# Kernel optimization log

Measured on AMD Instinct MI355X. Metric: run time of the kernel, lower is better.

Reference implementation:

```python
import jax, jax.numpy as jnp
import numpy as np

EPS = 1e-7
NUM_HEADS = 16

def _ln(x, g, b):
    m = jnp.mean(x, -1, keepdims=True)
    v = jnp.var(x, -1, keepdims=True)
    return (x - m) * jax.lax.rsqrt(v + EPS) * g + b

def _gelu(x):
    return jax.nn.gelu(x, approximate=False)  # torch nn.GELU default = exact erf

def _attn(x, qkv_w, qkv_b, pw, pb):
    B, N, C = x.shape
    D = C // NUM_HEADS
    qkv = (x @ qkv_w.T + qkv_b).reshape(B, N, 3, NUM_HEADS, D).transpose(2, 0, 3, 1, 4)
    q, k, v = qkv[0], qkv[1], qkv[2]
    a = jax.nn.softmax(jnp.einsum('bhnd,bhmd->bhnm', q, k) * (D ** -0.5), axis=-1)
    o = jnp.einsum('bhnm,bhmd->bhnd', a, v).transpose(0, 2, 1, 3).reshape(B, N, C)
    return o @ pw.T + pb

def _gcn(x, w, b, adj):
    # x: (B,C,J); w: (C*K,C) 1x1 conv, then einsum 'nkctv,kvw->nctw' with t==1
    K = adj.shape[0]
    B, C, J = x.shape
    y = jnp.einsum('bcj,oc->boj', x, w) + b[None, :, None]
    y = y.reshape(B, K, C, J)
    return jnp.einsum('bkcv,kvw->bcw', y, adj)

def _mlp(x, w1, b1, w2, b2):
    return _gelu(_gelu(x @ w1.T + b1) @ w2.T + b2)

def _lrsc(x, adj, l1g, l1b, l2g, l2b, g1w, g1b, g2w, g2b, m1w, m1b, m2w, m2b):
    x = x.transpose(0, 2, 1)                       # (B,C,J)
    res = x
    xn = _ln(x, l1g, l1b)                          # LayerNorm over J
    x = res + _mlp(xn, m1w, m1b, m2w, m2b) + _gcn(xn, g1w, g1b, adj)
    x = _ln(x.transpose(0, 2, 1), l2g, l2b).transpose(0, 2, 1)  # LayerNorm over C
    res = x
    x = res + _mlp(x, m1w, m1b, m2w, m2b) + _gcn(x, g2w, g2b, adj)
    return x.transpose(0, 2, 1)                    # (B,J,C)

def _gkpc(x, lg, lb, q1w, q1b, p1w, p1b, q2w, q2b, p2w, p2b):
    x = x + _attn(_ln(x, lg, lb), q1w, q1b, p1w, p1b)
    return _attn(_ln(x, lg, lb), q2w, q2b, p2w, p2b)  # note: no residual on second attn

def _forward(x, adj, ln1_g, ln1_b, ln2_g, ln2_b, gcn1_w, gcn1_b, gcn2_w, gcn2_b,
             mlp1_w1, mlp1_b1, mlp1_w2, mlp1_b2, attn_ln_g, attn_ln_b,
             qkv1_w, qkv1_b, proj1_w, proj1_b, qkv2_w, qkv2_b, proj2_w, proj2_b,
             tn_g, tn_b):
    L = ln1_g.shape[0]
    for i in range(L):
        # GG_ACM/RR_ACM/LCM are published as identity -> both 0.3/0.7 mixes equal x + gelu(x)
        xin = x + _gelu(x)
        x5 = _gkpc(xin, attn_ln_g[i], attn_ln_b[i], qkv1_w[i], qkv1_b[i],
                   proj1_w[i], proj1_b[i], qkv2_w[i], qkv2_b[i], proj2_w[i], proj2_b[i])
        x7 = _lrsc(xin, adj, ln1_g[i], ln1_b[i], ln2_g[i], ln2_b[i],
                   gcn1_w[i], gcn1_b[i], gcn2_w[i], gcn2_b[i],
                   mlp1_w1[i], mlp1_b1[i], mlp1_w2[i], mlp1_b2[i])
        x = x + x5 + x7
    return _ln(x, tn_g, tn_b)

def setup_inputs():
    B, V, C, K, L = 2048, 17, 512, 3, 3
    s = 0.05
    ks = jax.random.split(jax.random.key(0), 12)
    rn = lambda k, sh: jax.random.normal(k, sh, jnp.float32) * s
    return dict(
        x=jax.random.normal(ks[0], (B, V, C), jnp.float32),
        adj=jax.random.uniform(ks[1], (K, V, V), dtype=jnp.float32),
        ln1_g=jnp.ones((L, V), jnp.float32), ln1_b=jnp.zeros((L, V), jnp.float32),
        ln2_g=jnp.ones((L, C), jnp.float32), ln2_b=jnp.zeros((L, C), jnp.float32),
        gcn1_w=rn(ks[2], (L, C * K, C)), gcn1_b=jnp.zeros((L, C * K), jnp.float32),
        gcn2_w=rn(ks[3], (L, C * K, C)), gcn2_b=jnp.zeros((L, C * K), jnp.float32),
        mlp1_w1=rn(ks[4], (L, C, V)), mlp1_b1=jnp.zeros((L, C), jnp.float32),
        mlp1_w2=rn(ks[5], (L, V, C)), mlp1_b2=jnp.zeros((L, V), jnp.float32),
        attn_ln_g=jnp.ones((L, C), jnp.float32), attn_ln_b=jnp.zeros((L, C), jnp.float32),
        qkv1_w=rn(ks[6], (L, 3 * C, C)), qkv1_b=jnp.zeros((L, 3 * C), jnp.float32),
        proj1_w=rn(ks[7], (L, C, C)), proj1_b=jnp.zeros((L, C), jnp.float32),
        qkv2_w=rn(ks[8], (L, 3 * C, C)), qkv2_b=jnp.zeros((L, 3 * C), jnp.float32),
        proj2_w=rn(ks[9], (L, C, C)), proj2_b=jnp.zeros((L, C), jnp.float32),
        tn_g=jnp.ones((C,), jnp.float32), tn_b=jnp.zeros((C,), jnp.float32),
    )

def reference(x, adj, ln1_g, ln1_b, ln2_g, ln2_b, gcn1_w, gcn1_b, gcn2_w, gcn2_b,
              mlp1_w1, mlp1_b1, mlp1_w2, mlp1_b2, attn_ln_g, attn_ln_b,
              qkv1_w, qkv1_b, proj1_w, proj1_b, qkv2_w, qkv2_b, proj2_w, proj2_b,
              tn_g, tn_b):
    return _forward(x, adj, ln1_g, ln1_b, ln2_g, ln2_b, gcn1_w, gcn1_b, gcn2_w, gcn2_b,
                    mlp1_w1, mlp1_b1, mlp1_w2, mlp1_b2, attn_ln_g, attn_ln_b,
                    qkv1_w, qkv1_b, proj1_w, proj1_b, qkv2_w, qkv2_b, proj2_w, proj2_b,
                    tn_g, tn_b)
```

## Files before the change

kernel.cpp:

```cpp
#include <hip/hip_runtime.h>
#include <hip/hip_bf16.h>
#include <math.h>

#define Bn 2048
#define Vn 17
#define Cn 512
static const size_t NE = (size_t)Bn * Vn * Cn;
#define MROWS (Bn * Vn)

typedef __attribute__((ext_vector_type(8))) short bf16x8;
typedef __attribute__((ext_vector_type(4))) float f32x4;
typedef unsigned short u16;

__device__ __forceinline__ float u2f(u16 u) { return __uint_as_float(((unsigned)u) << 16); }
__device__ __forceinline__ u16 f2u(float f) {
    unsigned u = __float_as_uint(f);
    return (u16)((u + 0x7fffu + ((u >> 16) & 1u)) >> 16);
}
__device__ __forceinline__ float gelu_f(float x) {
    return 0.5f * x * (1.0f + erff(x * 0.70710678118654752f));
}
__device__ __forceinline__ float gelu_fast(float x) {
    float a = x * fmaf(x * x, 0.0713548162726f, 1.5957691216f);
    float e = __expf(-a);
    return x * __builtin_amdgcn_rcpf(1.0f + e);
}
__device__ __forceinline__ void gload16(const u16* g, u16* l) {
    __builtin_amdgcn_global_load_lds((const __attribute__((address_space(1))) void*)g,
                                     (__attribute__((address_space(3))) void*)l, 16, 0, 0);
}

__global__ void k_diag(float* __restrict__ o, float v, int n) {
    int i = blockIdx.x * 256 + threadIdx.x;
    if (i < n) o[i] = v;
}

__global__ void k_f2b(const float4* __restrict__ s, ushort4* __restrict__ d, int n4) {
    int i = blockIdx.x * 256 + threadIdx.x;
    if (i >= n4) return;
    float4 v = s[i];
    ushort4 o = {f2u(v.x), f2u(v.y), f2u(v.z), f2u(v.w)};
    d[i] = o;
}

__global__ void k_mpad(const float* __restrict__ W1, const float* __restrict__ W2,
                       u16* __restrict__ W1p, u16* __restrict__ W2b) {
    int t = blockIdx.x * 256 + threadIdx.x;
    if (t < 512 * 32) {
        int o = t >> 5, j = t & 31;
        W1p[t] = (j < 17) ? f2u(W1[o * 17 + j]) : (u16)0;
    }
    int t2 = t - 512 * 32;
    if (t2 >= 0 && t2 < 17 * 512) W2b[t2] = f2u(W2[t2]);
}

__global__ void k_xingelu(const float* __restrict__ X, u16* __restrict__ O, int n8) {
    int i = blockIdx.x * 256 + threadIdx.x;
    if (i >= n8) return;
    float4 a = *(const float4*)(X + (size_t)i * 8);
    float4 b = *(const float4*)(X + (size_t)i * 8 + 4);
    float v[8] = {a.x, a.y, a.z, a.w, b.x, b.y, b.z, b.w};
    bf16x8 r;
#pragma unroll
    for (int k = 0; k < 8; k++) r[k] = f2u(v[k] + gelu_f(v[k]));
    *(bf16x8*)(O + (size_t)i * 8) = r;
}

template <int F32IO>
__global__ __launch_bounds__(256) void k_ln_c(const void* __restrict__ Xv,
                                              const float* __restrict__ g,
                                              const float* __restrict__ bt,
                                              void* __restrict__ Ov, int nrows) {
    int row = blockIdx.x * 4 + (threadIdx.x >> 6);
    if (row >= nrows) return;
    int lane = threadIdx.x & 63;
    float vv[8];
    if (F32IO) {
        const float* xp = (const float*)Xv + (size_t)row * Cn + lane * 8;
        float4 v0 = *(const float4*)xp, v1 = *(const float4*)(xp + 4);
        vv[0] = v0.x; vv[1] = v0.y; vv[2] = v0.z; vv[3] = v0.w;
        vv[4] = v1.x; vv[5] = v1.y; vv[6] = v1.z; vv[7] = v1.w;
    } else {
        bf16x8 h = *(const bf16x8*)((const u16*)Xv + (size_t)row * Cn + lane * 8);
#pragma unroll
        for (int k = 0; k < 8; k++) vv[k] = u2f((u16)h[k]);
    }
    float s = 0.f, q = 0.f;
#pragma unroll
    for (int k = 0; k < 8; k++) { s += vv[k]; q = fmaf(vv[k], vv[k], q); }
#pragma unroll
    for (int o = 32; o; o >>= 1) { s += __shfl_xor(s, o); q += __shfl_xor(q, o); }
    float mean = s * (1.f / Cn);
    float var = q * (1.f / Cn) - mean * mean;
    float inv = 1.f / sqrtf(var + 1e-7f);
    int cb = lane * 8;
    if (F32IO) {
        float r[8];
#pragma unroll
        for (int k = 0; k < 8; k++) r[k] = (vv[k] - mean) * inv * g[cb + k] + bt[cb + k];
        float* op = (float*)Ov + (size_t)row * Cn + cb;
        *(float4*)op = make_float4(r[0], r[1], r[2], r[3]);
        *(float4*)(op + 4) = make_float4(r[4], r[5], r[6], r[7]);
    } else {
        bf16x8 r;
#pragma unroll
        for (int k = 0; k < 8; k++) r[k] = f2u((vv[k] - mean) * inv * g[cb + k] + bt[cb + k]);
        *(bf16x8*)((u16*)Ov + (size_t)row * Cn + cb) = r;
    }
}

__global__ __launch_bounds__(256) void k_ln_j(const u16* __restrict__ X,
                                              const float* __restrict__ g,
                                              const float* __restrict__ bt,
                                              u16* __restrict__ O) {
    int idx = blockIdx.x * 256 + threadIdx.x;
    int b = idx >> 9, c = idx & 511;
    const u16* xp = X + (size_t)b * Vn * Cn + c;
    float v[Vn];
    float s = 0.f;
#pragma unroll
    for (int j = 0; j < Vn; j++) { v[j] = u2f(xp[(size_t)j * Cn]); s += v[j]; }
    float mean = s * (1.f / Vn);
    float q = 0.f;
#pragma unroll
    for (int j = 0; j < Vn; j++) { float d = v[j] - mean; q = fmaf(d, d, q); }
    float inv = 1.f / sqrtf(q * (1.f / Vn) + 1e-7f);
    u16* op = O + (size_t)b * Vn * Cn + c;
#pragma unroll
    for (int j = 0; j < Vn; j++) op[(size_t)j * Cn] = f2u((v[j] - mean) * inv * g[j] + bt[j]);
}

template <int REMAP, int EPI>
__global__ __launch_bounds__(256) void k_gemm(const u16* __restrict__ A, const u16* __restrict__ W,
                                              const float* __restrict__ bias, u16* __restrict__ OutB,
                                              const u16* __restrict__ Res, float* __restrict__ Xf,
                                              int hbase, int shift) {
    constexpr int NT = REMAP ? 6 : 8;
    const int K = 512;
    int wave = threadIdx.x >> 6, lane = threadIdx.x & 63;
    int m0 = blockIdx.x * 128 + wave * 32;
    int nbase = blockIdx.y * (16 * NT);
    int r16 = lane & 15, kq = lane >> 4;
    int ld = REMAP ? (3 << shift) : 512;

    const u16* wp[NT];
    int wrow[NT];
#pragma unroll
    for (int nt = 0; nt < NT; nt++) {
        int n = nbase + nt * 16 + r16;
        int wr;
        if (REMAP) {
            int s = n >> shift, off = n & ((1 << shift) - 1);
            wr = (s << 9) + hbase + off;
        } else wr = n;
        wrow[nt] = wr;
        wp[nt] = W + (size_t)wr * K + kq * 8;
    }
    f32x4 acc[2][NT];
#pragma unroll
    for (int i = 0; i < 2; i++)
#pragma unroll
        for (int nt = 0; nt < NT; nt++) acc[i][nt] = (f32x4){0.f, 0.f, 0.f, 0.f};

    const u16* ap = A + (size_t)(m0 + r16) * K + kq * 8;
    for (int k0 = 0; k0 < K; k0 += 32) {
        bf16x8 a0 = *(const bf16x8*)(ap + k0);
        bf16x8 a1 = *(const bf16x8*)(ap + (size_t)16 * K + k0);
#pragma unroll
        for (int nt = 0; nt < NT; nt++) {
            bf16x8 bf = *(const bf16x8*)(wp[nt] + k0);
            acc[0][nt] = __builtin_amdgcn_mfma_f32_16x16x32_bf16(a0, bf, acc[0][nt], 0, 0, 0);
            acc[1][nt] = __builtin_amdgcn_mfma_f32_16x16x32_bf16(a1, bf, acc[1][nt], 0, 0, 0);
        }
    }
#pragma unroll
    for (int nt = 0; nt < NT; nt++) {
        float bv = bias[wrow[nt]];
        int n = nbase + nt * 16 + r16;
#pragma unroll
        for (int i = 0; i < 2; i++) {
#pragma unroll
            for (int r = 0; r < 4; r++) {
                size_t mb = (size_t)(m0 + i * 16 + kq * 4 + r);
                float v = acc[i][nt][r] + bv;
                if (EPI == 0) OutB[mb * ld + n] = f2u(v);
                else if (EPI == 1) { size_t o = mb * 512 + n; OutB[o] = f2u(v + u2f(Res[o])); }
                else { size_t o = mb * 512 + n; Xf[o] += v; }
            }
        }
    }
}

template <int EPI>
__global__ __launch_bounds__(256) void k_gemm2(const u16* __restrict__ A, const u16* __restrict__ W,
                                               const float* __restrict__ bias, u16* __restrict__ OutB,
                                               const u16* __restrict__ Res, float* __restrict__ Xf,
                                               int N) {
    __shared__ u16 As[128 * 64];
    __shared__ u16 Bs[128 * 64];
    const int K = 512;
    int tid = threadIdx.x;
    int wave = tid >> 6, lane = tid & 63;
    int m0 = blockIdx.x * 128, n0 = blockIdx.y * 128;
    int r16 = lane & 15, kq = lane >> 4;

    int srow = wave << 2;
    int lrow = lane >> 3;
    int lcol = (lane & 7) * 8;

    f32x4 acc[2][8];
#pragma unroll
    for (int i = 0; i < 2; i++)
#pragma unroll
        for (int j = 0; j < 8; j++) acc[i][j] = (f32x4){0.f, 0.f, 0.f, 0.f};

    const u16* aT = As + (wave * 32 + r16) * 64 + kq * 8;
    const u16* bT = Bs + r16 * 64 + kq * 8;

    for (int k0 = 0; k0 < K; k0 += 64) {
#pragma unroll
        for (int i = 0; i < 4; i++) {
            int rows = (srow + i) * 8 + lrow;
            gload16(A + (size_t)(m0 + rows) * K + k0 + lcol, (u16*)As + (srow + i) * 512);
            gload16(W + (size_t)(n0 + rows) * K + k0 + lcol, (u16*)Bs + (srow + i) * 512);
        }
        __syncthreads();
#pragma unroll
        for (int kk = 0; kk < 64; kk += 32) {
            bf16x8 af0 = *(const bf16x8*)(aT + kk);
            bf16x8 af1 = *(const bf16x8*)(aT + 16 * 64 + kk);
#pragma unroll
            for (int nt = 0; nt < 8; nt++) {
                bf16x8 bf = *(const bf16x8*)(bT + nt * 16 * 64 + kk);
                acc[0][nt] = __builtin_amdgcn_mfma_f32_16x16x32_bf16(af0, bf, acc[0][nt], 0, 0, 0);
                acc[1][nt] = __builtin_amdgcn_mfma_f32_16x16x32_bf16(af1, bf, acc[1][nt], 0, 0, 0);
            }
        }
        __syncthreads();
    }

    int mw = m0 + wave * 32;
#pragma unroll
    for (int nt = 0; nt < 8; nt++) {
        int n = n0 + nt * 16 + r16;
        float bv = bias[n];
#pragma unroll
        for (int i = 0; i < 2; i++) {
#pragma unroll
            for (int r = 0; r < 4; r++) {
                size_t mb = (size_t)(mw + i * 16 + kq * 4 + r);
                size_t o = mb * N + n;
                float v = acc[i][nt][r] + bv;
                if (EPI == 0) OutB[o] = f2u(v);
                else if (EPI == 1) OutB[o] = f2u(v + u2f(Res[o]));
                else Xf[o] += v;
            }
        }
    }
}

__global__ __launch_bounds__(256) void k_attn(const u16* __restrict__ Y, u16* __restrict__ T,
                                              int shift, int hgbase, int l2ch) {
    int wv = threadIdx.x >> 6, lane = threadIdx.x & 63;
    if (lane >= 34) return;
    int gw = blockIdx.x * 4 + wv;
    int which = (lane >= 17) ? 1 : 0;
    int j = lane - which * 17;
    int pid = gw * 2 + which;
    int b = pid >> l2ch;
    int hl = pid & ((1 << l2ch) - 1);
    int CW = 1 << shift;
    int row3 = 3 << shift;

    const u16* qb = Y + (size_t)(b * Vn + j) * row3 + hl * 32;
    float q[32];
#pragma unroll
    for (int d0 = 0; d0 < 32; d0 += 8) {
        bf16x8 h = *(const bf16x8*)(qb + d0);
#pragma unroll
        for (int d = 0; d < 8; d++) q[d0 + d] = u2f((u16)h[d]);
    }
    float sc[Vn];
    float mx = -1e30f;
#pragma unroll
    for (int kk = 0; kk < Vn; kk++) {
        const u16* kb = Y + (size_t)(b * Vn + kk) * row3 + CW + hl * 32;
        float s = 0.f;
#pragma unroll
        for (int d0 = 0; d0 < 32; d0 += 8) {
            bf16x8 h = *(const bf16x8*)(kb + d0);
#pragma unroll
            for (int d = 0; d < 8; d++) s = fmaf(q[d0 + d], u2f((u16)h[d]), s);
        }
        s *= 0.1767766952966369f;
        sc[kk] = s;
        mx = fmaxf(mx, s);
    }
    float sum = 0.f;
#pragma unroll
    for (int kk = 0; kk < Vn; kk++) { sc[kk] = __expf(sc[kk] - mx); sum += sc[kk]; }
    float inv = 1.f / sum;
    float o[32];
#pragma unroll
    for (int d = 0; d < 32; d++) o[d] = 0.f;
#pragma unroll
    for (int kk = 0; kk < Vn; kk++) {
        const u16* vb = Y + (size_t)(b * Vn + kk) * row3 + 2 * CW + hl * 32;
        float p = sc[kk] * inv;
#pragma unroll
        for (int d0 = 0; d0 < 32; d0 += 8) {
            bf16x8 h = *(const bf16x8*)(vb + d0);
#pragma unroll
            for (int d = 0; d < 8; d++) o[d0 + d] = fmaf(p, u2f((u16)h[d]), o[d0 + d]);
        }
    }
    u16* op = T + (size_t)(b * Vn + j) * Cn + hgbase + hl * 32;
#pragma unroll
    for (int d0 = 0; d0 < 32; d0 += 8) {
        bf16x8 r;
#pragma unroll
        for (int d = 0; d < 8; d++) r[d] = f2u(o[d0 + d]);
        *(bf16x8*)(op + d0) = r;
    }
}

template <int MODE>
__global__ __launch_bounds__(256) void k_agg(const u16* __restrict__ Y, const float* __restrict__ Adj,
                                             const u16* __restrict__ aux1, const u16* __restrict__ aux2,
                                             u16* __restrict__ OutB, float* __restrict__ Xf,
                                             int cbase, int shift) {
    __shared__ float adj_s[3][Vn][Vn];
    for (int t = threadIdx.x; t < 3 * Vn * Vn; t += 256) {
        int k = t / (Vn * Vn), r = t - k * Vn * Vn;
        adj_s[k][r / Vn][r % Vn] = Adj[t];
    }
    __syncthreads();
    int CW = 1 << shift;
    int idx = blockIdx.x * 256 + threadIdx.x;
    int b = idx >> shift, co = idx & (CW - 1);
    int c = cbase + co;
    int row3 = 3 << shift;
    float acc[Vn];
#pragma unroll
    for (int w = 0; w < Vn; w++) acc[w] = 0.f;
    const u16* yb = Y + (size_t)b * Vn * row3 + co;
#pragma unroll
    for (int k = 0; k < 3; k++)
#pragma unroll
        for (int v = 0; v < Vn; v++) {
            float y = u2f(yb[(size_t)v * row3 + k * CW]);
#pragma unroll
            for (int w = 0; w < Vn; w++) acc[w] = fmaf(y, adj_s[k][v][w], acc[w]);
        }
    size_t rb = (size_t)(b * Vn) * Cn + c;
#pragma unroll
    for (int w = 0; w < Vn; w++) {
        size_t o = rb + (size_t)w * Cn;
        float val = acc[w] + u2f(aux1[o]) + u2f(aux2[o]);
        if (MODE == 0) OutB[o] = f2u(val);
        else Xf[o] += val;
    }
}

__global__ __launch_bounds__(512) void k_mlp(const u16* __restrict__ X,
                                             const u16* __restrict__ W1p, const float* __restrict__ B1,
                                             const u16* __restrict__ W2b, const float* __restrict__ B2,
                                             u16* __restrict__ O) {
    __shared__ u16 Xs[256 * 40];
    __shared__ u16 Hs[256 * 40];
    int b = blockIdx.x >> 1;
    int cbase = (blockIdx.x & 1) << 8;
    int tid = threadIdx.x;

    for (int i = tid; i < 256 * 40 / 8; i += 512) ((float4*)Xs)[i] = make_float4(0.f, 0.f, 0.f, 0.f);
    __syncthreads();
    const u16* xb = X + (size_t)b * (Vn * Cn) + cbase;
    for (int i = tid; i < 17 * 256; i += 512) {
        int j = i >> 8, c = i & 255;
        Xs[c * 40 + j] = xb[j * Cn + c];
    }
    __syncthreads();

    int wave = tid >> 6, lane = tid & 63;
    int r16 = lane & 15, kq = lane >> 4;
    int crow = wave * 32;

    f32x4 acc2[2][2];
#pragma unroll
    for (int i = 0; i < 2; i++)
#pragma unroll
        for (int j = 0; j < 2; j++) acc2[i][j] = (f32x4){0.f, 0.f, 0.f, 0.f};

    const u16* xs0 = Xs + (crow + r16) * 40 + kq * 8;
    const u16* hs0 = Hs + (crow + r16) * 40 + kq * 8;

    for (int s = 0; s < 16; s++) {
        const u16* w1p = W1p + ((s * 32 + r16) << 5) + kq * 8;
        bf16x8 af0 = *(const bf16x8*)w1p;
        bf16x8 af1 = *(const bf16x8*)(w1p + 16 * 32);
        bf16x8 xf0 = *(const bf16x8*)xs0;
        bf16x8 xf1 = *(const bf16x8*)(xs0 + 16 * 40);
        f32x4 z = (f32x4){0.f, 0.f, 0.f, 0.f};
        f32x4 a00 = __builtin_amdgcn_mfma_f32_16x16x32_bf16(af0, xf0, z, 0, 0, 0);
        f32x4 a01 = __builtin_amdgcn_mfma_f32_16x16x32_bf16(af0, xf1, z, 0, 0, 0);
        f32x4 a10 = __builtin_amdgcn_mfma_f32_16x16x32_bf16(af1, xf0, z, 0, 0, 0);
        f32x4 a11 = __builtin_amdgcn_mfma_f32_16x16x32_bf16(af1, xf1, z, 0, 0, 0);
        const float* bp = B1 + s * 32 + kq * 4;
        float b0[4], b1v[4];
#pragma unroll
        for (int r = 0; r < 4; r++) { b0[r] = bp[r]; b1v[r] = bp[16 + r]; }
        {
            uint g[2];
            u16* hw;
#define STORE_H(ACC, NT, OT, BV)                                                        \
            {                                                                            \
                u16 q0 = f2u(gelu_fast(ACC[0] + BV[0]));                                 \
                u16 q1 = f2u(gelu_fast(ACC[1] + BV[1]));                                 \
                u16 q2 = f2u(gelu_fast(ACC[2] + BV[2]));                                 \
                u16 q3 = f2u(gelu_fast(ACC[3] + BV[3]));                                 \
                g[0] = (uint)q0 | ((uint)q1 << 16);                                      \
                g[1] = (uint)q2 | ((uint)q3 << 16);                                      \
                hw = Hs + (crow + NT * 16 + r16) * 40 + OT * 16 + kq * 4;                \
                *(uint2*)hw = make_uint2(g[0], g[1]);                                    \
            }
            STORE_H(a00, 0, 0, b0)
            STORE_H(a01, 1, 0, b0)
            STORE_H(a10, 0, 1, b1v)
            STORE_H(a11, 1, 1, b1v)
#undef STORE_H
        }
        __builtin_amdgcn_sched_barrier(0);
        bf16x8 h0 = *(const bf16x8*)hs0;
        bf16x8 h1 = *(const bf16x8*)(hs0 + 16 * 40);
        const u16* w2p = W2b + s * 32 + kq * 8;
        bf16x8 wf0 = *(const bf16x8*)(w2p + r16 * 512);
        bf16x8 wf1 = *(const bf16x8*)(w2p + 16 * 512);
        acc2[0][0] = __builtin_amdgcn_mfma_f32_16x16x32_bf16(h0, wf0, acc2[0][0], 0, 0, 0);
        acc2[0][1] = __builtin_amdgcn_mfma_f32_16x16x32_bf16(h0, wf1, acc2[0][1], 0, 0, 0);
        acc2[1][0] = __builtin_amdgcn_mfma_f32_16x16x32_bf16(h1, wf0, acc2[1][0], 0, 0, 0);
        acc2[1][1] = __builtin_amdgcn_mfma_f32_16x16x32_bf16(h1, wf1, acc2[1][1], 0, 0, 0);
    }

    u16* ob = O + (size_t)b * (Vn * Cn) + cbase;
#pragma unroll
    for (int nt = 0; nt < 2; nt++) {
        int cl = crow + nt * 16 + kq * 4;
#pragma unroll
        for (int n2 = 0; n2 < 2; n2++) {
            int w = n2 * 16 + r16;
            if (w < 17) {
                float bb = B2[w];
                u16 q0 = f2u(gelu_fast(acc2[nt][n2][0] + bb));
                u16 q1 = f2u(gelu_fast(acc2[nt][n2][1] + bb));
                u16 q2 = f2u(gelu_fast(acc2[nt][n2][2] + bb));
                u16 q3 = f2u(gelu_fast(acc2[nt][n2][3] + bb));
                *(uint2*)(ob + (size_t)w * Cn + cl) =
                    make_uint2((uint)q0 | ((uint)q1 << 16), (uint)q2 | ((uint)q3 << 16));
            }
        }
    }
}

extern "C" void kernel_launch(void* const* d_in, const int* in_sizes, int n_in,
                              void* d_out, int out_size, void* d_ws, size_t ws_size,
                              hipStream_t stream) {
    (void)in_sizes; (void)n_in; (void)out_size;
    typedef const float* fp;
    fp x_in = (fp)d_in[0];
    fp adj = (fp)d_in[1];
    fp ln1_g = (fp)d_in[2], ln1_b = (fp)d_in[3];
    fp ln2_g = (fp)d_in[4], ln2_b = (fp)d_in[5];
    fp gcn1_w = (fp)d_in[6], gcn1_b = (fp)d_in[7];
    fp gcn2_w = (fp)d_in[8], gcn2_b = (fp)d_in[9];
    fp m1w = (fp)d_in[10], m1b = (fp)d_in[11];
    fp m2w = (fp)d_in[12], m2b = (fp)d_in[13];
    fp aln_g = (fp)d_in[14], aln_b = (fp)d_in[15];
    fp qkv1_w = (fp)d_in[16], qkv1_b = (fp)d_in[17];
    fp p1w = (fp)d_in[18], p1b = (fp)d_in[19];
    fp qkv2_w = (fp)d_in[20], qkv2_b = (fp)d_in[21];
    fp p2w = (fp)d_in[22], p2b = (fp)d_in[23];
    fp tn_g = (fp)d_in[24], tn_b = (fp)d_in[25];

    const size_t NE2 = NE * 2;
    const size_t WSCR_SZ = (size_t)1536 * 512 * 2;
    const size_t MPAD_SZ = (size_t)(512 * 32 + 17 * 512) * 2;

    int CH = 0;
    for (int ch = 16; ch >= 1; ch >>= 1) {
        size_t need = 3 * NE2 + WSCR_SZ + MPAD_SZ + (size_t)MROWS * 96 * ch * 2 + 1024;
        if (need <= ws_size) { CH = ch; break; }
    }
    if (!CH) {
        k_diag<<<(int)((NE + 255) / 256), 256, 0, stream>>>((float*)d_out, (float)ws_size, (int)NE);
        return;
    }
    const int l2ch = __builtin_ctz(CH);
    const int shift = 5 + l2ch;
    const int NCH = 16 / CH;
    const bool FAST = (CH == 16);

    char* p = (char*)d_ws;
    u16* XIN = (u16*)p;  p += NE2;
    u16* T1 = (u16*)p;   p += NE2;
    u16* T2 = (u16*)p;   p += NE2;
    u16* YCH = (u16*)p;  p += (size_t)MROWS * 96 * CH * 2;
    u16* WSCR = (u16*)p; p += WSCR_SZ;
    u16* MPAD1 = (u16*)p;
    u16* MPAD2 = MPAD1 + 512 * 32;

    float* X = (float*)d_out;
    hipMemcpyAsync(X, x_in, NE * 4, hipMemcpyDeviceToDevice, stream);

    const int G8 = (int)(NE / 8 / 256);
    const int GLN = MROWS / 4;
    const int GBC = Bn * Cn / 256;
    const int GATT = (Bn << l2ch) / 8;
    const int GAGG = (Bn << shift) / 256;
    const dim3 GEMM_C(MROWS / 128, CH);
    const dim3 GEMM_P(MROWS / 128, 4);
    const dim3 GEMM_QF(MROWS / 128, 12);
    const int CV_QKV = (int)(1536 * 512 / 4 / 256);
    const int CV_P = (int)(512 * 512 / 4 / 256);

    for (int i = 0; i < 3; i++) {
        fp q1w = qkv1_w + (size_t)i * 1536 * 512, q1b = qkv1_b + i * 1536;
        fp q2w = qkv2_w + (size_t)i * 1536 * 512, q2b = qkv2_b + i * 1536;
        fp g1w = gcn1_w + (size_t)i * 1536 * 512, g1b = gcn1_b + i * 1536;
        fp g2w = gcn2_w + (size_t)i * 1536 * 512, g2b = gcn2_b + i * 1536;
        fp pw1 = p1w + (size_t)i * 512 * 512, pb1 = p1b + i * Cn;
        fp pw2 = p2w + (size_t)i * 512 * 512, pb2 = p2b + i * Cn;
        fp alg = aln_g + i * Cn, alb = aln_b + i * Cn;
        fp l1g = ln1_g + i * Vn, l1b_ = ln1_b + i * Vn;
        fp l2g = ln2_g + i * Cn, l2b_ = ln2_b + i * Cn;
        fp w1 = m1w + (size_t)i * Cn * Vn, b1 = m1b + i * Cn;
        fp w2 = m2w + (size_t)i * Vn * Cn, b2 = m2b + i * Vn;

        k_xingelu<<<G8, 256, 0, stream>>>(X, XIN, (int)(NE / 8));
        k_mpad<<<98, 256, 0, stream>>>(w1, w2, MPAD1, MPAD2);

        k_ln_c<0><<<GLN, 256, 0, stream>>>(XIN, alg, alb, T1, MROWS);
        k_f2b<<<CV_QKV, 256, 0, stream>>>((const float4*)q1w, (ushort4*)WSCR, 1536 * 512 / 4);
        if (FAST) {
            k_gemm2<0><<<GEMM_QF, 256, 0, stream>>>(T1, WSCR, q1b, YCH, nullptr, nullptr, 1536);
            k_attn<<<GATT, 256, 0, stream>>>(YCH, T2, shift, 0, l2ch);
        } else {
            for (int hg = 0; hg < NCH; hg++) {
                k_gemm<1, 0><<<GEMM_C, 256, 0, stream>>>(T1, WSCR, q1b, YCH, nullptr, nullptr, hg << shift, shift);
                k_attn<<<GATT, 256, 0, stream>>>(YCH, T2, shift, hg << shift, l2ch);
            }
        }
        k_f2b<<<CV_P, 256, 0, stream>>>((const float4*)pw1, (ushort4*)WSCR, 512 * 512 / 4);
        if (FAST) k_gemm2<1><<<GEMM_P, 256, 0, stream>>>(T2, WSCR, pb1, T1, XIN, nullptr, 512);
        else k_gemm<0, 1><<<GEMM_P, 256, 0, stream>>>(T2, WSCR, pb1, T1, XIN, nullptr, 0, 0);
        k_ln_c<0><<<GLN, 256, 0, stream>>>(T1, alg, alb, T2, MROWS);
        k_f2b<<<CV_QKV, 256, 0, stream>>>((const float4*)q2w, (ushort4*)WSCR, 1536 * 512 / 4);
        if (FAST) {
            k_gemm2<0><<<GEMM_QF, 256, 0, stream>>>(T2, WSCR, q2b, YCH, nullptr, nullptr, 1536);
            k_attn<<<GATT, 256, 0, stream>>>(YCH, T1, shift, 0, l2ch);
        } else {
            for (int hg = 0; hg < NCH; hg++) {
                k_gemm<1, 0><<<GEMM_C, 256, 0, stream>>>(T2, WSCR, q2b, YCH, nullptr, nullptr, hg << shift, shift);
                k_attn<<<GATT, 256, 0, stream>>>(YCH, T1, shift, hg << shift, l2ch);
            }
        }
        k_f2b<<<CV_P, 256, 0, stream>>>((const float4*)pw2, (ushort4*)WSCR, 512 * 512 / 4);
        if (FAST) k_gemm2<2><<<GEMM_P, 256, 0, stream>>>(T1, WSCR, pb2, nullptr, nullptr, X, 512);
        else k_gemm<0, 2><<<GEMM_P, 256, 0, stream>>>(T1, WSCR, pb2, nullptr, nullptr, X, 0, 0);

        k_ln_j<<<GBC, 256, 0, stream>>>(XIN, l1g, l1b_, T1);
        k_mlp<<<Bn * 2, 512, 0, stream>>>(T1, MPAD1, b1, MPAD2, b2, T2);
        k_f2b<<<CV_QKV, 256, 0, stream>>>((const float4*)g1w, (ushort4*)WSCR, 1536 * 512 / 4);
        if (FAST) {
            k_gemm2<0><<<GEMM_QF, 256, 0, stream>>>(T1, WSCR, g1b, YCH, nullptr, nullptr, 1536);
            k_agg<0><<<GAGG, 256, 0, stream>>>(YCH, adj, XIN, T2, XIN, nullptr, 0, shift);
        } else {
            for (int cc = 0; cc < NCH; cc++) {
                k_gemm<1, 0><<<GEMM_C, 256, 0, stream>>>(T1, WSCR, g1b, YCH, nullptr, nullptr, cc << shift, shift);
                k_agg<0><<<GAGG, 256, 0, stream>>>(YCH, adj, XIN, T2, XIN, nullptr, cc << shift, shift);
            }
        }
        k_ln_c<0><<<GLN, 256, 0, stream>>>(XIN, l2g, l2b_, T1, MROWS);
        k_mlp<<<Bn * 2, 512, 0, stream>>>(T1, MPAD1, b1, MPAD2, b2, T2);
        k_f2b<<<CV_QKV, 256, 0, stream>>>((const float4*)g2w, (ushort4*)WSCR, 1536 * 512 / 4);
        if (FAST) {
            k_gemm2<0><<<GEMM_QF, 256, 0, stream>>>(T1, WSCR, g2b, YCH, nullptr, nullptr, 1536);
            k_agg<1><<<GAGG, 256, 0, stream>>>(YCH, adj, T1, T2, nullptr, X, 0, shift);
        } else {
            for (int cc = 0; cc < NCH; cc++) {
                k_gemm<1, 0><<<GEMM_C, 256, 0, stream>>>(T1, WSCR, g2b, YCH, nullptr, nullptr, cc << shift, shift);
                k_agg<1><<<GAGG, 256, 0, stream>>>(YCH, adj, T1, T2, nullptr, X, cc << shift, shift);
            }
        }
    }

    k_ln_c<1><<<GLN, 256, 0, stream>>>(X, tn_g, tn_b, X, MROWS);
}
```

Baseline: 4.081 ms.

## Keep MLP hidden in registers, swizzle GEMM block order, cheaper packed GELU

The MLP kernel no longer stages the GELU hidden activations through shared memory. The first MFMA's outputs are fed straight into the second GEMM as 16x16x16 operands, the bias is folded into the accumulator init, and a packed bf16 convert is used. GEMM2 blocks are remapped with an XCD-style swizzle (bid&7) so neighbouring tiles share L2 on the same die. GELU uses a raw v_exp_f32 with constants prescaled for exp2, and W2 is padded to 32 rows. The risks are more MFMA instructions, precision changes from the raw exp, and the swizzle assuming the grid size divides by 8.

```diff
diff --git a/kernel.cpp b/kernel.cpp
--- a/kernel.cpp
+++ b/kernel.cpp
@@ -9,7 +9,9 @@
 #define MROWS (Bn * Vn)
 
 typedef __attribute__((ext_vector_type(8))) short bf16x8;
+typedef __attribute__((ext_vector_type(4))) short bf16x4;
 typedef __attribute__((ext_vector_type(4))) float f32x4;
+typedef __attribute__((ext_vector_type(2))) unsigned int u32x2;
 typedef unsigned short u16;
 
 __device__ __forceinline__ float u2f(u16 u) { return __uint_as_float(((unsigned)u) << 16); }
@@ -20,10 +22,23 @@
 __device__ __forceinline__ float gelu_f(float x) {
     return 0.5f * x * (1.0f + erff(x * 0.70710678118654752f));
 }
+__device__ __forceinline__ float exp2_raw(float x) {
+    float r; asm("v_exp_f32 %0, %1" : "=v"(r) : "v"(x)); return r;
+}
 __device__ __forceinline__ float gelu_fast(float x) {
-    float a = x * fmaf(x * x, 0.0713548162726f, 1.5957691216f);
-    float e = __expf(-a);
-    return x * __builtin_amdgcn_rcpf(1.0f + e);
+    float b = x * fmaf(x * x, -0.10294348f, -2.30220820f);
+    return x * __builtin_amdgcn_rcpf(1.0f + exp2_raw(b));
+}
+__device__ __forceinline__ unsigned cvtpk(float lo, float hi) {
+    unsigned r; asm("v_cvt_pk_bf16_f32 %0, %1, %2" : "=v"(r) : "v"(lo), "v"(hi)); return r;
+}
+__device__ __forceinline__ bf16x4 gelupk(f32x4 v) {
+    u32x2 t = {cvtpk(gelu_fast(v[0]), gelu_fast(v[1])), cvtpk(gelu_fast(v[2]), gelu_fast(v[3]))};
+    return __builtin_bit_cast(bf16x4, t);
+}
+__device__ __forceinline__ f32x4 mfma16(bf16x4 a, bf16x4 b, f32x4 c) {
+    asm("v_mfma_f32_16x16x16_bf16 %0, %1, %2, %0" : "+v"(c) : "v"(a), "v"(b));
+    return c;
 }
 __device__ __forceinline__ void gload16(const u16* g, u16* l) {
     __builtin_amdgcn_global_load_lds((const __attribute__((address_space(1))) void*)g,
@@ -44,14 +59,16 @@
 }
 
 __global__ void k_mpad(const float* __restrict__ W1, const float* __restrict__ W2,
-                       u16* __restrict__ W1p, u16* __restrict__ W2b) {
+                       u16* __restrict__ W1p, u16* __restrict__ W2p) {
     int t = blockIdx.x * 256 + threadIdx.x;
     if (t < 512 * 32) {
         int o = t >> 5, j = t & 31;
         W1p[t] = (j < 17) ? f2u(W1[o * 17 + j]) : (u16)0;
-    }
-    int t2 = t - 512 * 32;
-    if (t2 >= 0 && t2 < 17 * 512) W2b[t2] = f2u(W2[t2]);
+    } else {
+        int t2 = t - 512 * 32;
+        int w = t2 >> 9;
+        W2p[t2] = (w < 17) ? f2u(W2[t2]) : (u16)0;
+    }
 }
 
 __global__ void k_xingelu(const float* __restrict__ X, u16* __restrict__ O, int n8) {
@@ -191,7 +208,7 @@
     }
 }
 
-template <int EPI>
+template <int EPI, int NY>
 __global__ __launch_bounds__(256) void k_gemm2(const u16* __restrict__ A, const u16* __restrict__ W,
                                                const float* __restrict__ bias, u16* __restrict__ OutB,
                                                const u16* __restrict__ Res, float* __restrict__ Xf,
@@ -201,7 +218,10 @@
     const int K = 512;
     int tid = threadIdx.x;
     int wave = tid >> 6, lane = tid & 63;
-    int m0 = blockIdx.x * 128, n0 = blockIdx.y * 128;
+    int cpx = gridDim.x >> 3;
+    int bid = blockIdx.x;
+    int swz = (bid & 7) * cpx + (bid >> 3);
+    int m0 = (swz / NY) * 128, n0 = (swz % NY) * 128;
     int r16 = lane & 15, kq = lane >> 4;
 
     int srow = wave << 2;
@@ -364,15 +384,16 @@
 
 __global__ __launch_bounds__(512) void k_mlp(const u16* __restrict__ X,
                                              const u16* __restrict__ W1p, const float* __restrict__ B1,
-                                             const u16* __restrict__ W2b, const float* __restrict__ B2,
+                                             const u16* __restrict__ W2p, const float* __restrict__ B2,
                                              u16* __restrict__ O) {
     __shared__ u16 Xs[256 * 40];
-    __shared__ u16 Hs[256 * 40];
+    __shared__ float B1s[512];
     int b = blockIdx.x >> 1;
     int cbase = (blockIdx.x & 1) << 8;
     int tid = threadIdx.x;
 
     for (int i = tid; i < 256 * 40 / 8; i += 512) ((float4*)Xs)[i] = make_float4(0.f, 0.f, 0.f, 0.f);
+    if (tid < 128) ((float4*)B1s)[tid] = ((const float4*)B1)[tid];
     __syncthreads();
     const u16* xb = X + (size_t)b * (Vn * Cn) + cbase;
     for (int i = tid; i < 17 * 256; i += 512) {
@@ -385,78 +406,59 @@
     int r16 = lane & 15, kq = lane >> 4;
     int crow = wave * 32;
 
+    bf16x8 xf0 = *(const bf16x8*)(Xs + (crow + r16) * 40 + kq * 8);
+    bf16x8 xf1 = *(const bf16x8*)(Xs + (crow + 16 + r16) * 40 + kq * 8);
+
     f32x4 acc2[2][2];
 #pragma unroll
     for (int i = 0; i < 2; i++)
 #pragma unroll
         for (int j = 0; j < 2; j++) acc2[i][j] = (f32x4){0.f, 0.f, 0.f, 0.f};
-
-    const u16* xs0 = Xs + (crow + r16) * 40 + kq * 8;
-    const u16* hs0 = Hs + (crow + r16) * 40 + kq * 8;
 
     for (int s = 0; s < 16; s++) {
         const u16* w1p = W1p + ((s * 32 + r16) << 5) + kq * 8;
         bf16x8 af0 = *(const bf16x8*)w1p;
         bf16x8 af1 = *(const bf16x8*)(w1p + 16 * 32);
-        bf16x8 xf0 = *(const bf16x8*)xs0;
-        bf16x8 xf1 = *(const bf16x8*)(xs0 + 16 * 40);
-        f32x4 z = (f32x4){0.f, 0.f, 0.f, 0.f};
-        f32x4 a00 = __builtin_amdgcn_mfma_f32_16x16x32_bf16(af0, xf0, z, 0, 0, 0);
-        f32x4 a01 = __builtin_amdgcn_mfma_f32_16x16x32_bf16(af0, xf1, z, 0, 0, 0);
-        f32x4 a10 = __builtin_amdgcn_mfma_f32_16x16x32_bf16(af1, xf0, z, 0, 0, 0);
-        f32x4 a11 = __builtin_amdgcn_mfma_f32_16x16x32_bf16(af1, xf1, z, 0, 0, 0);
-        const float* bp = B1 + s * 32 + kq * 4;
-        float b0[4], b1v[4];
-#pragma unroll
-        for (int r = 0; r < 4; r++) { b0[r] = bp[r]; b1v[r] = bp[16 + r]; }
-        {
-            uint g[2];
-            u16* hw;
-#define STORE_H(ACC, NT, OT, BV)                                                        \
-            {                                                                            \
-                u16 q0 = f2u(gelu_fast(ACC[0] + BV[0]));                                 \
-                u16 q1 = f2u(gelu_fast(ACC[1] + BV[1]));                                 \
-                u16 q2 = f2u(gelu_fast(ACC[2] + BV[2]));                                 \
-                u16 q3 = f2u(gelu_fast(ACC[3] + BV[3]));                                 \
-                g[0] = (uint)q0 | ((uint)q1 << 16);                                      \
-                g[1] = (uint)q2 | ((uint)q3 << 16);                                      \
-                hw = Hs + (crow + NT * 16 + r16) * 40 + OT * 16 + kq * 4;                \
-                *(uint2*)hw = make_uint2(g[0], g[1]);                                    \
-            }
-            STORE_H(a00, 0, 0, b0)
-            STORE_H(a01, 1, 0, b0)
-            STORE_H(a10, 0, 1, b1v)
-            STORE_H(a11, 1, 1, b1v)
-#undef STORE_H
-        }
-        __builtin_amdgcn_sched_barrier(0);
-        bf16x8 h0 = *(const bf16x8*)hs0;
-        bf16x8 h1 = *(const bf16x8*)(hs0 + 16 * 40);
-        const u16* w2p = W2b + s * 32 + kq * 8;
-        bf16x8 wf0 = *(const bf16x8*)(w2p + r16 * 512);
-        bf16x8 wf1 = *(const bf16x8*)(w2p + 16 * 512);
-        acc2[0][0] = __builtin_amdgcn_mfma_f32_16x16x32_bf16(h0, wf0, acc2[0][0], 0, 0, 0);
-        acc2[0][1] = __builtin_amdgcn_mfma_f32_16x16x32_bf16(h0, wf1, acc2[0][1], 0, 0, 0);
-        acc2[1][0] = __builtin_amdgcn_mfma_f32_16x16x32_bf16(h1, wf0, acc2[1][0], 0, 0, 0);
-        acc2[1][1] = __builtin_amdgcn_mfma_f32_16x16x32_bf16(h1, wf1, acc2[1][1], 0, 0, 0);
+        f32x4 bi0 = *(const f32x4*)(B1s + s * 32 + kq * 4);
+        f32x4 bi1 = *(const f32x4*)(B1s + s * 32 + 16 + kq * 4);
+        f32x4 a00 = __builtin_amdgcn_mfma_f32_16x16x32_bf16(af0, xf0, bi0, 0, 0, 0);
+        f32x4 a01 = __builtin_amdgcn_mfma_f32_16x16x32_bf16(af0, xf1, bi0, 0, 0, 0);
+        f32x4 a10 = __builtin_amdgcn_mfma_f32_16x16x32_bf16(af1, xf0, bi1, 0, 0, 0);
+        f32x4 a11 = __builtin_amdgcn_mfma_f32_16x16x32_bf16(af1, xf1, bi1, 0, 0, 0);
+        bf16x4 p00 = gelupk(a00);
+        bf16x4 p01 = gelupk(a01);
+        bf16x4 p10 = gelupk(a10);
+        bf16x4 p11 = gelupk(a11);
+        const u16* w2p = W2p + (size_t)r16 * 512 + s * 32 + kq * 4;
+        bf16x4 wb00 = *(const bf16x4*)(w2p);
+        bf16x4 wb01 = *(const bf16x4*)(w2p + 16);
+        bf16x4 wb10 = *(const bf16x4*)(w2p + 16 * 512);
+        bf16x4 wb11 = *(const bf16x4*)(w2p + 16 * 512 + 16);
+        acc2[0][0] = mfma16(p00, wb00, acc2[0][0]);
+        acc2[0][0] = mfma16(p10, wb01, acc2[0][0]);
+        acc2[1][0] = mfma16(p01, wb00, acc2[1][0]);
+        acc2[1][0] = mfma16(p11, wb01, acc2[1][0]);
+        acc2[0][1] = mfma16(p00, wb10, acc2[0][1]);
+        acc2[0][1] = mfma16(p10, wb11, acc2[0][1]);
+        acc2[1][1] = mfma16(p01, wb10, acc2[1][1]);
+        acc2[1][1] = mfma16(p11, wb11, acc2[1][1]);
     }
 
     u16* ob = O + (size_t)b * (Vn * Cn) + cbase;
-#pragma unroll
-    for (int nt = 0; nt < 2; nt++) {
-        int cl = crow + nt * 16 + kq * 4;
-#pragma unroll
-        for (int n2 = 0; n2 < 2; n2++) {
-            int w = n2 * 16 + r16;
-            if (w < 17) {
-                float bb = B2[w];
-                u16 q0 = f2u(gelu_fast(acc2[nt][n2][0] + bb));
-                u16 q1 = f2u(gelu_fast(acc2[nt][n2][1] + bb));
-                u16 q2 = f2u(gelu_fast(acc2[nt][n2][2] + bb));
-                u16 q3 = f2u(gelu_fast(acc2[nt][n2][3] + bb));
-                *(uint2*)(ob + (size_t)w * Cn + cl) =
-                    make_uint2((uint)q0 | ((uint)q1 << 16), (uint)q2 | ((uint)q3 << 16));
-            }
+    float bb0 = B2[r16];
+#pragma unroll
+    for (int cg = 0; cg < 2; cg++) {
+        int cl = crow + cg * 16 + kq * 4;
+        f32x4 v = acc2[cg][0];
+        uint2 pk = make_uint2(cvtpk(gelu_fast(v[0] + bb0), gelu_fast(v[1] + bb0)),
+                              cvtpk(gelu_fast(v[2] + bb0), gelu_fast(v[3] + bb0)));
+        *(uint2*)(ob + (size_t)r16 * Cn + cl) = pk;
+        if (r16 == 0) {
+            float bb1 = B2[16];
+            f32x4 w = acc2[cg][1];
+            uint2 pk1 = make_uint2(cvtpk(gelu_fast(w[0] + bb1), gelu_fast(w[1] + bb1)),
+                                   cvtpk(gelu_fast(w[2] + bb1), gelu_fast(w[3] + bb1)));
+            *(uint2*)(ob + (size_t)16 * Cn + cl) = pk1;
         }
     }
 }
@@ -483,7 +485,7 @@
 
     const size_t NE2 = NE * 2;
     const size_t WSCR_SZ = (size_t)1536 * 512 * 2;
-    const size_t MPAD_SZ = (size_t)(512 * 32 + 17 * 512) * 2;
+    const size_t MPAD_SZ = (size_t)(512 * 32 + 32 * 512) * 2;
 
     int CH = 0;
     for (int ch = 16; ch >= 1; ch >>= 1) {
@@ -518,9 +520,10 @@
     const int GAGG = (Bn << shift) / 256;
     const dim3 GEMM_C(MROWS / 128, CH);
     const dim3 GEMM_P(MROWS / 128, 4);
-    const dim3 GEMM_QF(MROWS / 128, 12);
     const int CV_QKV = (int)(1536 * 512 / 4 / 256);
     const int CV_P = (int)(512 * 512 / 4 / 256);
+    const int GQF = (MROWS / 128) * 12;
+    const int GPF = (MROWS / 128) * 4;
 
     for (int i = 0; i < 3; i++) {
         fp q1w = qkv1_w + (size_t)i * 1536 * 512, q1b = qkv1_b + i * 1536;
@@ -536,12 +539,12 @@
         fp w2 = m2w + (size_t)i * Vn * Cn, b2 = m2b + i * Vn;
 
         k_xingelu<<<G8, 256, 0, stream>>>(X, XIN, (int)(NE / 8));
-        k_mpad<<<98, 256, 0, stream>>>(w1, w2, MPAD1, MPAD2);
+        k_mpad<<<128, 256, 0, stream>>>(w1, w2, MPAD1, MPAD2);
 
         k_ln_c<0><<<GLN, 256, 0, stream>>>(XIN, alg, alb, T1, MROWS);
         k_f2b<<<CV_QKV, 256, 0, stream>>>((const float4*)q1w, (ushort4*)WSCR, 1536 * 512 / 4);
         if (FAST) {
-            k_gemm2<0><<<GEMM_QF, 256, 0, stream>>>(T1, WSCR, q1b, YCH, nullptr, nullptr, 1536);
+            k_gemm2<0, 12><<<GQF, 256, 0, stream>>>(T1, WSCR, q1b, YCH, nullptr, nullptr, 1536);
             k_attn<<<GATT, 256, 0, stream>>>(YCH, T2, shift, 0, l2ch);
         } else {
             for (int hg = 0; hg < NCH; hg++) {
@@ -550,12 +553,12 @@
             }
         }
         k_f2b<<<CV_P, 256, 0, stream>>>((const float4*)pw1, (ushort4*)WSCR, 512 * 512 / 4);
-        if (FAST) k_gemm2<1><<<GEMM_P, 256, 0, stream>>>(T2, WSCR, pb1, T1, XIN, nullptr, 512);
+        if (FAST) k_gemm2<1, 4><<<GPF, 256, 0, stream>>>(T2, WSCR, pb1, T1, XIN, nullptr, 512);
         else k_gemm<0, 1><<<GEMM_P, 256, 0, stream>>>(T2, WSCR, pb1, T1, XIN, nullptr, 0, 0);
         k_ln_c<0><<<GLN, 256, 0, stream>>>(T1, alg, alb, T2, MROWS);
         k_f2b<<<CV_QKV, 256, 0, stream>>>((const float4*)q2w, (ushort4*)WSCR, 1536 * 512 / 4);
         if (FAST) {
-            k_gemm2<0><<<GEMM_QF, 256, 0, stream>>>(T2, WSCR, q2b, YCH, nullptr, nullptr, 1536);
+            k_gemm2<0, 12><<<GQF, 256, 0, stream>>>(T2, WSCR, q2b, YCH, nullptr, nullptr, 1536);
             k_attn<<<GATT, 256, 0, stream>>>(YCH, T1, shift, 0, l2ch);
         } else {
             for (int hg = 0; hg < NCH; hg++) {
@@ -564,14 +567,14 @@
             }
         }
         k_f2b<<<CV_P, 256, 0, stream>>>((const float4*)pw2, (ushort4*)WSCR, 512 * 512 / 4);
-        if (FAST) k_gemm2<2><<<GEMM_P, 256, 0, stream>>>(T1, WSCR, pb2, nullptr, nullptr, X, 512);
+        if (FAST) k_gemm2<2, 4><<<GPF, 256, 0, stream>>>(T1, WSCR, pb2, nullptr, nullptr, X, 512);
         else k_gemm<0, 2><<<GEMM_P, 256, 0, stream>>>(T1, WSCR, pb2, nullptr, nullptr, X, 0, 0);
 
         k_ln_j<<<GBC, 256, 0, stream>>>(XIN, l1g, l1b_, T1);
         k_mlp<<<Bn * 2, 512, 0, stream>>>(T1, MPAD1, b1, MPAD2, b2, T2);
         k_f2b<<<CV_QKV, 256, 0, stream>>>((const float4*)g1w, (ushort4*)WSCR, 1536 * 512 / 4);
         if (FAST) {
-            k_gemm2<0><<<GEMM_QF, 256, 0, stream>>>(T1, WSCR, g1b, YCH, nullptr, nullptr, 1536);
+            k_gemm2<0, 12><<<GQF, 256, 0, stream>>>(T1, WSCR, g1b, YCH, nullptr, nullptr, 1536);
             k_agg<0><<<GAGG, 256, 0, stream>>>(YCH, adj, XIN, T2, XIN, nullptr, 0, shift);
         } else {
             for (int cc = 0; cc < NCH; cc++) {
@@ -583,7 +586,7 @@
         k_mlp<<<Bn * 2, 512, 0, stream>>>(T1, MPAD1, b1, MPAD2, b2, T2);
         k_f2b<<<CV_QKV, 256, 0, stream>>>((const float4*)g2w, (ushort4*)WSCR, 1536 * 512 / 4);
         if (FAST) {
-            k_gemm2<0><<<GEMM_QF, 256, 0, stream>>>(T1, WSCR, g2b, YCH, nullptr, nullptr, 1536);
+            k_gemm2<0, 12><<<GQF, 256, 0, stream>>>(T1, WSCR, g2b, YCH, nullptr, nullptr, 1536);
             k_agg<1><<<GAGG, 256, 0, stream>>>(YCH, adj, T1, T2, nullptr, X, 0, shift);
         } else {
             for (int cc = 0; cc < NCH; cc++) {
```

After: 4.397 ms. 1.08x slower.
